# Kernel tuning notes

Measured on AMD Instinct MI355X. Metric: run time of the kernel, lower is better.

The kernel has to match this reference:

```python
import jax, jax.numpy as jnp
import numpy as np

N_NODES = 20000
N_EDGES = 640000
K_CHEB = 20


def setup_inputs() -> dict:
    key = jax.random.key(0)
    ks = jax.random.split(key, 8)
    x = jax.random.normal(ks[0], (128, N_NODES, 1), dtype=jnp.float32)
    rows = jax.random.randint(ks[1], (N_EDGES,), 0, N_NODES, dtype=jnp.int32)
    cols = jax.random.randint(ks[2], (N_EDGES,), 0, N_NODES, dtype=jnp.int32)
    # rescaled-Laplacian-like values, small scale so the K=20 recursion stays bounded
    vals = jax.random.normal(ks[3], (N_EDGES,), dtype=jnp.float32) * 0.05
    W_gc = jax.random.normal(ks[4], (K_CHEB, 10), dtype=jnp.float32) * 0.1
    b_gc = jnp.zeros((10,), dtype=jnp.float32)
    W_fc = jax.random.normal(ks[5], (N_NODES * 10, 10), dtype=jnp.float32) * 0.01
    b_fc = jnp.zeros((10,), dtype=jnp.float32)
    return {"x": x, "rows": rows, "cols": cols, "vals": vals,
            "W_gc": W_gc, "b_gc": b_gc, "W_fc": W_fc, "b_fc": b_fc}


def reference(x, rows, cols, vals, W_gc, b_gc, W_fc, b_fc):
    B, N, Fin = x.shape  # Fin == 1
    x0 = x[..., 0].T  # [N, B]

    def spmm(t):  # sparse L @ t via edge-list scatter-add, t: [N, B]
        return jax.ops.segment_sum(vals[:, None] * t[cols], rows, num_segments=N)

    # Chebyshev recursion: T0 = x, T1 = L x, Tk = 2 L T_{k-1} - T_{k-2}
    Ts = [x0, spmm(x0)]
    for _ in range(K_CHEB - 2):
        Ts.append(2.0 * spmm(Ts[-1]) - Ts[-2])
    Xt = jnp.stack(Ts, axis=-1)  # [N, B, K]

    gc = jnp.einsum('nbk,kf->bnf', Xt, W_gc) + b_gc  # [B, N, 10]
    gc = jax.nn.relu(gc)
    flat = gc.reshape(B, N * 10)
    h = jax.nn.relu(flat @ W_fc + b_fc)  # [B, 10]
    return jax.nn.softmax(h, axis=1)
```

## Files before the change

kernel.cpp:

```cpp
#include <hip/hip_runtime.h>
#include <hip/hip_bf16.h>
#include <hip/hip_fp16.h>
#include <math.h>


#define NF 10
#define KCHEB 20
#define BCG 64
#define COFF16 (KCHEB * BCG)

typedef unsigned int u32;


__global__ void init_kernel(int* counts, float* h_part, const float* __restrict__ W_gc,
                            float* __restrict__ WgT, int N, int H) {
    int i = blockIdx.x * blockDim.x + threadIdx.x;
    if (i < N) counts[i] = 0;
    if (i < H) h_part[i] = 0.f;
    if (i < KCHEB * NF) WgT[(i % NF) * KCHEB + (i / NF)] = W_gc[i];
}

__global__ void hist_kernel(const int* __restrict__ rows, int* __restrict__ counts, int E) {
    int e = blockIdx.x * blockDim.x + threadIdx.x;
    if (e < E) atomicAdd(&counts[rows[e]], 1);
}

#define SCAN_THREADS 1024
__global__ void scan_kernel(const int* __restrict__ counts, int* __restrict__ row_start,
                            int* __restrict__ cursor, int N) {
    __shared__ int sh[SCAN_THREADS];
    int t = threadIdx.x;
    int CH = (N + SCAN_THREADS - 1) / SCAN_THREADS;
    int base = t * CH;
    int sum = 0;
    for (int i = 0; i < CH; ++i) {
        int idx = base + i;
        sum += (idx < N) ? counts[idx] : 0;
    }
    sh[t] = sum;
    __syncthreads();
    for (int off = 1; off < SCAN_THREADS; off <<= 1) {
        int v = (t >= off) ? sh[t - off] : 0;
        __syncthreads();
        sh[t] += v;
        __syncthreads();
    }
    int run = (t == 0) ? 0 : sh[t - 1];
    for (int i = 0; i < CH; ++i) {
        int idx = base + i;
        if (idx < N) {
            int v = counts[idx];
            row_start[idx] = run;
            cursor[idx] = run;
            run += v;
        }
    }
    if (t == SCAN_THREADS - 1) row_start[N] = run;
}

__global__ void scatter_kernel(const int* __restrict__ rows, const int* __restrict__ cols,
                               const float* __restrict__ vals, int* __restrict__ cursor,
                               int2* __restrict__ csr, int E) {
    int e = blockIdx.x * blockDim.x + threadIdx.x;
    if (e >= E) return;
    int p = atomicAdd(&cursor[rows[e]], 1);
    csr[p] = make_int2(cols[e] * COFF16, __float_as_int(vals[e]));
}


__global__ void transpose_kernel(const float* __restrict__ x, __half* __restrict__ X16,
                                 float* __restrict__ C32, int N, int ntiles, int b0s) {
    __shared__ float tile[BCG][65];
    int tid = threadIdx.x;
    int g = blockIdx.x / ntiles;
    int ti = blockIdx.x - g * ntiles;
    int n0 = ti * 64;
#pragma unroll
    for (int p = 0; p < 16; ++p) {
        int idx = p * 256 + tid;
        int row = idx >> 6;
        int col = idx & 63;
        if (n0 + col < N)
            tile[row][col] = x[(size_t)(b0s + g * BCG + row) * N + n0 + col];
    }
    __syncthreads();
#pragma unroll
    for (int p = 0; p < 16; ++p) {
        int idx = p * 256 + tid;
        int nloc = idx >> 6;
        int bb = idx & 63;
        int n = n0 + nloc;
        if (n < N) {
            float v = tile[bb][nloc];
            X16[(size_t)(g * N + n) * COFF16 + bb] = __float2half_rn(v);
            C32[((size_t)(g * 2 + 0) * N + n) * BCG + bb] = v;
        }
    }
}


__global__ __launch_bounds__(256)
void spmm_kernel(__half* __restrict__ X16, float* __restrict__ C32,
                 const int* __restrict__ row_start, const int2* __restrict__ csr,
                 int N, int xpcShift, int subsPerChunk,
                 int kIn, int kOut, float alpha, float beta) {
    int xcd = blockIdx.x & 7;
    int chunk = xcd >> xpcShift;
    int xpcMask = (1 << xpcShift) - 1;
    int sub = (blockIdx.x >> 3) * (1 << xpcShift) + (xcd & xpcMask);
    if (sub >= subsPerChunk) return;
    int tid = threadIdx.x;
    int ln = tid >> 3;
    int bq = tid & 7;
    int n = sub * 32 + ln;
    if (n >= N) return;
    int s = row_start[n];
    int e = row_start[n + 1];

    const __half* gin = X16 + (size_t)chunk * N * COFF16;
    int koff = kIn * BCG + bq * 8;
    int bo = bq * 8;
    float acc[8];
#pragma unroll
    for (int q = 0; q < 8; ++q) acc[q] = 0.f;

    int i = s;
    for (; i + 4 <= e; i += 4) {
        int2 p0 = csr[i], p1 = csr[i + 1], p2 = csr[i + 2], p3 = csr[i + 3];
        uint4 u0 = *(const uint4*)(gin + p0.x + koff);
        uint4 u1 = *(const uint4*)(gin + p1.x + koff);
        uint4 u2 = *(const uint4*)(gin + p2.x + koff);
        uint4 u3 = *(const uint4*)(gin + p3.x + koff);
        float v0 = __int_as_float(p0.y), v1 = __int_as_float(p1.y);
        float v2 = __int_as_float(p2.y), v3 = __int_as_float(p3.y);
        {
            float2 f0 = __half22float2(*(__half2*)&u0.x), f1 = __half22float2(*(__half2*)&u0.y);
            float2 f2 = __half22float2(*(__half2*)&u0.z), f3 = __half22float2(*(__half2*)&u0.w);
            acc[0] += v0 * f0.x; acc[1] += v0 * f0.y; acc[2] += v0 * f1.x; acc[3] += v0 * f1.y;
            acc[4] += v0 * f2.x; acc[5] += v0 * f2.y; acc[6] += v0 * f3.x; acc[7] += v0 * f3.y;
        }
        {
            float2 f0 = __half22float2(*(__half2*)&u1.x), f1 = __half22float2(*(__half2*)&u1.y);
            float2 f2 = __half22float2(*(__half2*)&u1.z), f3 = __half22float2(*(__half2*)&u1.w);
            acc[0] += v1 * f0.x; acc[1] += v1 * f0.y; acc[2] += v1 * f1.x; acc[3] += v1 * f1.y;
            acc[4] += v1 * f2.x; acc[5] += v1 * f2.y; acc[6] += v1 * f3.x; acc[7] += v1 * f3.y;
        }
        {
            float2 f0 = __half22float2(*(__half2*)&u2.x), f1 = __half22float2(*(__half2*)&u2.y);
            float2 f2 = __half22float2(*(__half2*)&u2.z), f3 = __half22float2(*(__half2*)&u2.w);
            acc[0] += v2 * f0.x; acc[1] += v2 * f0.y; acc[2] += v2 * f1.x; acc[3] += v2 * f1.y;
            acc[4] += v2 * f2.x; acc[5] += v2 * f2.y; acc[6] += v2 * f3.x; acc[7] += v2 * f3.y;
        }
        {
            float2 f0 = __half22float2(*(__half2*)&u3.x), f1 = __half22float2(*(__half2*)&u3.y);
            float2 f2 = __half22float2(*(__half2*)&u3.z), f3 = __half22float2(*(__half2*)&u3.w);
            acc[0] += v3 * f0.x; acc[1] += v3 * f0.y; acc[2] += v3 * f1.x; acc[3] += v3 * f1.y;
            acc[4] += v3 * f2.x; acc[5] += v3 * f2.y; acc[6] += v3 * f3.x; acc[7] += v3 * f3.y;
        }
    }
    for (; i < e; ++i) {
        int2 p0 = csr[i];
        uint4 u0 = *(const uint4*)(gin + p0.x + koff);
        float v0 = __int_as_float(p0.y);
        float2 f0 = __half22float2(*(__half2*)&u0.x), f1 = __half22float2(*(__half2*)&u0.y);
        float2 f2 = __half22float2(*(__half2*)&u0.z), f3 = __half22float2(*(__half2*)&u0.w);
        acc[0] += v0 * f0.x; acc[1] += v0 * f0.y; acc[2] += v0 * f1.x; acc[3] += v0 * f1.y;
        acc[4] += v0 * f2.x; acc[5] += v0 * f2.y; acc[6] += v0 * f3.x; acc[7] += v0 * f3.y;
    }

    float* cslot = C32 + ((size_t)(chunk * 2 + (kOut & 1)) * N + n) * BCG + bo;
    float o[8];
#pragma unroll
    for (int q = 0; q < 8; ++q) o[q] = alpha * acc[q];
    if (beta != 0.f) {
        const float4 pv0 = *(const float4*)(cslot);
        const float4 pv1 = *(const float4*)(cslot + 4);
        o[0] += beta * pv0.x; o[1] += beta * pv0.y; o[2] += beta * pv0.z; o[3] += beta * pv0.w;
        o[4] += beta * pv1.x; o[5] += beta * pv1.y; o[6] += beta * pv1.z; o[7] += beta * pv1.w;
    }
    *(float4*)(cslot)     = make_float4(o[0], o[1], o[2], o[3]);
    *(float4*)(cslot + 4) = make_float4(o[4], o[5], o[6], o[7]);
    __half* o16 = X16 + (size_t)(chunk * N + n) * COFF16 + kOut * BCG + bo;
    uint4 h4;
    __half2 h01 = __floats2half2_rn(o[0], o[1]);
    __half2 h23 = __floats2half2_rn(o[2], o[3]);
    __half2 h45 = __floats2half2_rn(o[4], o[5]);
    __half2 h67 = __floats2half2_rn(o[6], o[7]);
    h4.x = *(u32*)&h01; h4.y = *(u32*)&h23; h4.z = *(u32*)&h45; h4.w = *(u32*)&h67;
    *(uint4*)o16 = h4;
}


__global__ __launch_bounds__(1024, 8)
void proj_fc_kernel(const __half* __restrict__ X16,
                    const float* __restrict__ WgT,
                    const float* __restrict__ b_gc,
                    const float* __restrict__ W_fc,
                    float* __restrict__ h_part,
                    int N, int b0s, int G) {
    __shared__ float sRed[BCG * 11];
    int tid = threadIdx.x;
    for (int i = tid; i < BCG * 11; i += 1024) sRed[i] = 0.f;
    __syncthreads();

    int g = blockIdx.x % G;
    int bidx = blockIdx.x / G;
    int nblk = gridDim.x / G;

    int bb = tid & (BCG - 1);
    int wv = __builtin_amdgcn_readfirstlane(tid >> 6);

    float h_loc[NF];
#pragma unroll
    for (int f = 0; f < NF; ++f) h_loc[f] = 0.f;

    const __half* chunkBase = X16 + (size_t)g * N * COFF16;
    int ngroups = (N + 15) / 16;
    for (int grp = bidx; grp < ngroups; grp += nblk) {
        int n = grp * 16 + wv;
        if (n < N) {
            float xt[KCHEB];
            const __half* xp = chunkBase + (size_t)n * COFF16 + bb;
#pragma unroll
            for (int k = 0; k < KCHEB; ++k) xt[k] = __half2float(xp[k * BCG]);

            const float* wfBase = W_fc + (size_t)n * (NF * NF);
#pragma unroll 1
            for (int j = 0; j < NF; ++j) {
                const float* wg = WgT + j * KCHEB;
                float gc = b_gc[j];
#pragma unroll
                for (int k = 0; k < KCHEB; ++k) gc += wg[k] * xt[k];
                gc = fmaxf(gc, 0.f);
                const float* wf = wfBase + j * NF;
#pragma unroll
                for (int f = 0; f < NF; ++f) h_loc[f] += gc * wf[f];
            }
        }
    }
#pragma unroll
    for (int f = 0; f < NF; ++f) atomicAdd(&sRed[bb * 11 + f], h_loc[f]);
    __syncthreads();
    for (int i = tid; i < BCG * NF; i += 1024) {
        int rb = i / NF;
        int rf = i - rb * NF;
        atomicAdd(&h_part[(size_t)(b0s + g * BCG + rb) * NF + rf], sRed[rb * 11 + rf]);
    }
}


__global__ void softmax_kernel(const float* __restrict__ h_part, const float* __restrict__ b_fc,
                               float* __restrict__ out, int B) {
    int b = blockIdx.x * blockDim.x + threadIdx.x;
    if (b >= B) return;
    float v[NF];
    float m = -1e30f;
#pragma unroll
    for (int f = 0; f < NF; ++f) {
        float t = fmaxf(h_part[b * NF + f] + b_fc[f], 0.f);
        v[f] = t;
        m = fmaxf(m, t);
    }
    float s = 0.f;
#pragma unroll
    for (int f = 0; f < NF; ++f) { v[f] = expf(v[f] - m); s += v[f]; }
    float inv = 1.f / s;
#pragma unroll
    for (int f = 0; f < NF; ++f) out[b * NF + f] = v[f] * inv;
}


extern "C" void kernel_launch(void* const* d_in, const int* in_sizes, int n_in,
                              void* d_out, int out_size, void* d_ws, size_t ws_size,
                              hipStream_t stream) {
    const float* x    = (const float*)d_in[0];
    const int*   rows = (const int*)d_in[1];
    const int*   cols = (const int*)d_in[2];
    const float* vals = (const float*)d_in[3];
    const float* W_gc = (const float*)d_in[4];
    const float* b_gc = (const float*)d_in[5];
    const float* W_fc = (const float*)d_in[6];
    const float* b_fc = (const float*)d_in[7];
    float* out = (float*)d_out;

    const int E = in_sizes[1];
    const int N = in_sizes[6] / (NF * NF);
    const int B = in_sizes[0] / N;

    char* p = (char*)d_ws;
    int* counts    = (int*)p;   p += sizeof(int) * (size_t)N;
    int* row_start = (int*)p;   p += sizeof(int) * (size_t)(N + 1);
    int* cursor    = (int*)p;   p += sizeof(int) * (size_t)N;
    p = (char*)(((size_t)p + 15) & ~(size_t)15);
    int2* csr      = (int2*)p;  p += sizeof(int2) * (size_t)E;
    float* h_part  = (float*)p; p += sizeof(float) * (size_t)B * NF;
    p = (char*)(((size_t)p + 15) & ~(size_t)15);
    float* WgT     = (float*)p; p += sizeof(float) * (size_t)(NF * KCHEB);
    size_t fixed = (size_t)(p - (char*)d_ws);
    fixed = (fixed + 255) & ~(size_t)255;

    size_t perChunk16 = (size_t)N * COFF16 * sizeof(__half);
    size_t perCarry   = (size_t)2 * N * BCG * sizeof(float);
    int G = (B >= 2 * BCG) ? 2 : 1;
    while (G > 1 && fixed + (size_t)G * (perChunk16 + perCarry) > ws_size) G >>= 1;
    __half* X16 = (__half*)((char*)d_ws + fixed);
    size_t x16b = ((size_t)G * perChunk16 + 255) & ~(size_t)255;
    float* C32 = (float*)((char*)d_ws + fixed + x16b);
    int xpcShift = (G == 2) ? 2 : 3;
    int BT = G * BCG;
    int nsc = B / BT;

    {
        int H = B * NF;
        int cov = (N > H) ? N : H;
        init_kernel<<<(cov + 255) / 256, 256, 0, stream>>>(counts, h_part, W_gc, WgT, N, H);
        hist_kernel<<<(E + 255) / 256, 256, 0, stream>>>(rows, counts, E);
        scan_kernel<<<1, SCAN_THREADS, 0, stream>>>(counts, row_start, cursor, N);
        scatter_kernel<<<(E + 255) / 256, 256, 0, stream>>>(rows, cols, vals, cursor, csr, E);
    }

    int ntiles = (N + 63) / 64;
    int subsPerChunk = (N + 31) / 32;
    int xpc = 1 << xpcShift;
    int gridSpmm = 8 * ((subsPerChunk + xpc - 1) / xpc);

    for (int c = 0; c < nsc; ++c) {
        int b0s = c * BT;
        transpose_kernel<<<G * ntiles, 256, 0, stream>>>(x, X16, C32, N, ntiles, b0s);
        for (int k = 1; k < KCHEB; ++k) {
            float alpha = (k == 1) ? 1.f : 2.f;
            float beta  = (k == 1) ? 0.f : -1.f;
            spmm_kernel<<<gridSpmm, 256, 0, stream>>>(
                X16, C32, row_start, csr, N, xpcShift, subsPerChunk,
                k - 1, k, alpha, beta);
        }
        proj_fc_kernel<<<256 * G, 1024, 0, stream>>>(X16, WgT, b_gc, W_fc, h_part, N, b0s, G);
    }

    softmax_kernel<<<1, 128, 0, stream>>>(h_part, b_fc, out, B);
}
```

Measured before the change: 597.5 us.

## Split SpMM into column-partitioned gather and partial-sum reduce kernels

The CSR is rebuilt so that edges are bucketed by column range as well as by row. This lets each XCD gather only from its own slice of the source features, shrinking the per-XCD gather working set for better L2 locality. Each gather writes per-slice partial sums to a new fp32 buffer with nontemporal stores. A second kernel then sums the slices and applies the Chebyshev alpha/beta update. The cost is an extra kernel launch per recursion step, plus writing and reading that partial buffer, which is several times the output size.

```diff
diff --git a/kernel.cpp b/kernel.cpp
--- a/kernel.cpp
+++ b/kernel.cpp
@@ -10,32 +10,37 @@
 #define COFF16 (KCHEB * BCG)
 
 typedef unsigned int u32;
+typedef float v4f __attribute__((ext_vector_type(4)));
 
 
 __global__ void init_kernel(int* counts, float* h_part, const float* __restrict__ W_gc,
-                            float* __restrict__ WgT, int N, int H) {
+                            float* __restrict__ WgT, int N4, int H) {
     int i = blockIdx.x * blockDim.x + threadIdx.x;
-    if (i < N) counts[i] = 0;
+    if (i < N4) counts[i] = 0;
     if (i < H) h_part[i] = 0.f;
     if (i < KCHEB * NF) WgT[(i % NF) * KCHEB + (i / NF)] = W_gc[i];
 }
 
-__global__ void hist_kernel(const int* __restrict__ rows, int* __restrict__ counts, int E) {
+__global__ void hist_kernel(const int* __restrict__ rows, const int* __restrict__ cols,
+                            int* __restrict__ counts, int E, int N, int QS) {
     int e = blockIdx.x * blockDim.x + threadIdx.x;
-    if (e < E) atomicAdd(&counts[rows[e]], 1);
+    if (e < E) {
+        int q = cols[e] / QS;
+        atomicAdd(&counts[q * N + rows[e]], 1);
+    }
 }
 
 #define SCAN_THREADS 1024
 __global__ void scan_kernel(const int* __restrict__ counts, int* __restrict__ row_start,
-                            int* __restrict__ cursor, int N) {
+                            int* __restrict__ cursor, int N4) {
     __shared__ int sh[SCAN_THREADS];
     int t = threadIdx.x;
-    int CH = (N + SCAN_THREADS - 1) / SCAN_THREADS;
+    int CH = (N4 + SCAN_THREADS - 1) / SCAN_THREADS;
     int base = t * CH;
     int sum = 0;
     for (int i = 0; i < CH; ++i) {
         int idx = base + i;
-        sum += (idx < N) ? counts[idx] : 0;
+        sum += (idx < N4) ? counts[idx] : 0;
     }
     sh[t] = sum;
     __syncthreads();
@@ -48,23 +53,25 @@
     int run = (t == 0) ? 0 : sh[t - 1];
     for (int i = 0; i < CH; ++i) {
         int idx = base + i;
-        if (idx < N) {
+        if (idx < N4) {
             int v = counts[idx];
             row_start[idx] = run;
             cursor[idx] = run;
             run += v;
         }
     }
-    if (t == SCAN_THREADS - 1) row_start[N] = run;
+    if (t == SCAN_THREADS - 1) row_start[N4] = run;
 }
 
 __global__ void scatter_kernel(const int* __restrict__ rows, const int* __restrict__ cols,
                                const float* __restrict__ vals, int* __restrict__ cursor,
-                               int2* __restrict__ csr, int E) {
+                               int2* __restrict__ csr, int E, int N, int QS) {
     int e = blockIdx.x * blockDim.x + threadIdx.x;
     if (e >= E) return;
-    int p = atomicAdd(&cursor[rows[e]], 1);
-    csr[p] = make_int2(cols[e] * COFF16, __float_as_int(vals[e]));
+    int col = cols[e];
+    int q = col / QS;
+    int p = atomicAdd(&cursor[q * N + rows[e]], 1);
+    csr[p] = make_int2(col * COFF16, __float_as_int(vals[e]));
 }
 
 
@@ -100,33 +107,32 @@
 
 
 __global__ __launch_bounds__(256)
-void spmm_kernel(__half* __restrict__ X16, float* __restrict__ C32,
-                 const int* __restrict__ row_start, const int2* __restrict__ csr,
-                 int N, int xpcShift, int subsPerChunk,
-                 int kIn, int kOut, float alpha, float beta) {
+void gather_kernel(const __half* __restrict__ X16, float* __restrict__ P,
+                   const int* __restrict__ row_start4, const int2* __restrict__ csr4,
+                   int N, int kIn, int nqMask, int nqSh, int gMask, int hSh, int twSh) {
     int xcd = blockIdx.x & 7;
-    int chunk = xcd >> xpcShift;
-    int xpcMask = (1 << xpcShift) - 1;
-    int sub = (blockIdx.x >> 3) * (1 << xpcShift) + (xcd & xpcMask);
-    if (sub >= subsPerChunk) return;
+    int sub = blockIdx.x >> 3;
+    int q = xcd & nqMask;
+    int c = (xcd >> nqSh) & gMask;
+    int h = xcd >> hSh;
     int tid = threadIdx.x;
     int ln = tid >> 3;
     int bq = tid & 7;
-    int n = sub * 32 + ln;
-    if (n >= N) return;
-    int s = row_start[n];
-    int e = row_start[n + 1];
-
-    const __half* gin = X16 + (size_t)chunk * N * COFF16;
+    int r = ((sub << twSh) + h) * 32 + ln;
+    if (r >= N) return;
+    int vr = q * N + r;
+    int s = row_start4[vr];
+    int e = row_start4[vr + 1];
+
+    const __half* gin = X16 + (size_t)c * N * COFF16;
     int koff = kIn * BCG + bq * 8;
-    int bo = bq * 8;
     float acc[8];
 #pragma unroll
-    for (int q = 0; q < 8; ++q) acc[q] = 0.f;
+    for (int t = 0; t < 8; ++t) acc[t] = 0.f;
 
     int i = s;
     for (; i + 4 <= e; i += 4) {
-        int2 p0 = csr[i], p1 = csr[i + 1], p2 = csr[i + 2], p3 = csr[i + 3];
+        int2 p0 = csr4[i], p1 = csr4[i + 1], p2 = csr4[i + 2], p3 = csr4[i + 3];
         uint4 u0 = *(const uint4*)(gin + p0.x + koff);
         uint4 u1 = *(const uint4*)(gin + p1.x + koff);
         uint4 u2 = *(const uint4*)(gin + p2.x + koff);
@@ -159,7 +165,7 @@
         }
     }
     for (; i < e; ++i) {
-        int2 p0 = csr[i];
+        int2 p0 = csr4[i];
         uint4 u0 = *(const uint4*)(gin + p0.x + koff);
         float v0 = __int_as_float(p0.y);
         float2 f0 = __half22float2(*(__half2*)&u0.x), f1 = __half22float2(*(__half2*)&u0.y);
@@ -168,10 +174,47 @@
         acc[4] += v0 * f2.x; acc[5] += v0 * f2.y; acc[6] += v0 * f3.x; acc[7] += v0 * f3.y;
     }
 
-    float* cslot = C32 + ((size_t)(chunk * 2 + (kOut & 1)) * N + n) * BCG + bo;
+    float* pp = P + ((size_t)((c << nqSh) + q) * N + r) * BCG + bq * 8;
+    v4f a0 = { acc[0], acc[1], acc[2], acc[3] };
+    v4f a1 = { acc[4], acc[5], acc[6], acc[7] };
+    __builtin_nontemporal_store(a0, (v4f*)pp);
+    __builtin_nontemporal_store(a1, (v4f*)(pp + 4));
+}
+
+
+__global__ __launch_bounds__(256)
+void reduce_kernel(__half* __restrict__ X16, float* __restrict__ C32,
+                   const float* __restrict__ P,
+                   int N, int QS, int NQ, int nqMask, int nqSh, int gMask, int hSh, int twSh,
+                   int kOut, float alpha, float beta) {
+    int xcd = blockIdx.x & 7;
+    int sub = blockIdx.x >> 3;
+    int q = xcd & nqMask;
+    int c = (xcd >> nqSh) & gMask;
+    int h = xcd >> hSh;
+    int tid = threadIdx.x;
+    int ln = tid >> 3;
+    int bq = tid & 7;
+    int r = q * QS + ((sub << twSh) + h) * 32 + ln;
+    int rend = (q + 1) * QS; if (rend > N) rend = N;
+    if (r >= rend) return;
+    int bo = bq * 8;
+
+    float acc[8];
+#pragma unroll
+    for (int t = 0; t < 8; ++t) acc[t] = 0.f;
+    for (int qq = 0; qq < NQ; ++qq) {
+        const float* pp = P + ((size_t)((c << nqSh) + qq) * N + r) * BCG + bo;
+        v4f a0 = __builtin_nontemporal_load((const v4f*)pp);
+        v4f a1 = __builtin_nontemporal_load((const v4f*)(pp + 4));
+        acc[0] += a0.x; acc[1] += a0.y; acc[2] += a0.z; acc[3] += a0.w;
+        acc[4] += a1.x; acc[5] += a1.y; acc[6] += a1.z; acc[7] += a1.w;
+    }
+
+    float* cslot = C32 + ((size_t)(c * 2 + (kOut & 1)) * N + r) * BCG + bo;
     float o[8];
 #pragma unroll
-    for (int q = 0; q < 8; ++q) o[q] = alpha * acc[q];
+    for (int t = 0; t < 8; ++t) o[t] = alpha * acc[t];
     if (beta != 0.f) {
         const float4 pv0 = *(const float4*)(cslot);
         const float4 pv1 = *(const float4*)(cslot + 4);
@@ -180,7 +223,7 @@
     }
     *(float4*)(cslot)     = make_float4(o[0], o[1], o[2], o[3]);
     *(float4*)(cslot + 4) = make_float4(o[4], o[5], o[6], o[7]);
-    __half* o16 = X16 + (size_t)(chunk * N + n) * COFF16 + kOut * BCG + bo;
+    __half* o16 = X16 + (size_t)(c * N + r) * COFF16 + kOut * BCG + bo;
     uint4 h4;
     __half2 h01 = __floats2half2_rn(o[0], o[1]);
     __half2 h23 = __floats2half2_rn(o[2], o[3]);
@@ -269,6 +312,8 @@
     for (int f = 0; f < NF; ++f) out[b * NF + f] = v[f] * inv;
 }
 
+
+static inline int ilog2i(int v) { int s = 0; while ((1 << s) < v) ++s; return s; }
 
 extern "C" void kernel_launch(void* const* d_in, const int* in_sizes, int n_in,
                               void* d_out, int out_size, void* d_ws, size_t ws_size,
@@ -288,9 +333,9 @@
     const int B = in_sizes[0] / N;
 
     char* p = (char*)d_ws;
-    int* counts    = (int*)p;   p += sizeof(int) * (size_t)N;
-    int* row_start = (int*)p;   p += sizeof(int) * (size_t)(N + 1);
-    int* cursor    = (int*)p;   p += sizeof(int) * (size_t)N;
+    int* counts    = (int*)p;   p += sizeof(int) * (size_t)(8 * N);
+    int* row_start = (int*)p;   p += sizeof(int) * (size_t)(8 * N + 1);
+    int* cursor    = (int*)p;   p += sizeof(int) * (size_t)(8 * N);
     p = (char*)(((size_t)p + 15) & ~(size_t)15);
     int2* csr      = (int2*)p;  p += sizeof(int2) * (size_t)E;
     float* h_part  = (float*)p; p += sizeof(float) * (size_t)B * NF;
@@ -301,28 +346,47 @@
 
     size_t perChunk16 = (size_t)N * COFF16 * sizeof(__half);
     size_t perCarry   = (size_t)2 * N * BCG * sizeof(float);
+    size_t perP       = (size_t)N * BCG * sizeof(float);
+
     int G = (B >= 2 * BCG) ? 2 : 1;
-    while (G > 1 && fixed + (size_t)G * (perChunk16 + perCarry) > ws_size) G >>= 1;
+    int NQ = (G == 2) ? 2 : 8;
+    while (fixed + (size_t)G * (perChunk16 + perCarry) + (size_t)G * NQ * perP > ws_size) {
+        if (G == 2) { G = 1; NQ = 8; }
+        else if (NQ > 1) { NQ >>= 1; }
+        else break;
+    }
     __half* X16 = (__half*)((char*)d_ws + fixed);
     size_t x16b = ((size_t)G * perChunk16 + 255) & ~(size_t)255;
     float* C32 = (float*)((char*)d_ws + fixed + x16b);
-    int xpcShift = (G == 2) ? 2 : 3;
+    size_t c32b = ((size_t)G * perCarry + 255) & ~(size_t)255;
+    float* P = (float*)((char*)d_ws + fixed + x16b + c32b);
+
     int BT = G * BCG;
     int nsc = B / BT;
+    int QS = (N + NQ - 1) / NQ;
+    int N4 = NQ * N;
+    int TW = 8 / (G * NQ);
+    int nqSh = ilog2i(NQ);
+    int gSh  = ilog2i(G);
+    int twSh = ilog2i(TW);
+    int hSh  = nqSh + gSh;
+    int nqMask = NQ - 1;
+    int gMask  = G - 1;
 
     {
         int H = B * NF;
-        int cov = (N > H) ? N : H;
-        init_kernel<<<(cov + 255) / 256, 256, 0, stream>>>(counts, h_part, W_gc, WgT, N, H);
-        hist_kernel<<<(E + 255) / 256, 256, 0, stream>>>(rows, counts, E);
-        scan_kernel<<<1, SCAN_THREADS, 0, stream>>>(counts, row_start, cursor, N);
-        scatter_kernel<<<(E + 255) / 256, 256, 0, stream>>>(rows, cols, vals, cursor, csr, E);
+        int cov = (N4 > H) ? N4 : H;
+        init_kernel<<<(cov + 255) / 256, 256, 0, stream>>>(counts, h_part, W_gc, WgT, N4, H);
+        hist_kernel<<<(E + 255) / 256, 256, 0, stream>>>(rows, cols, counts, E, N, QS);
+        scan_kernel<<<1, SCAN_THREADS, 0, stream>>>(counts, row_start, cursor, N4);
+        scatter_kernel<<<(E + 255) / 256, 256, 0, stream>>>(rows, cols, vals, cursor, csr, E, N, QS);
     }
 
     int ntiles = (N + 63) / 64;
-    int subsPerChunk = (N + 31) / 32;
-    int xpc = 1 << xpcShift;
-    int gridSpmm = 8 * ((subsPerChunk + xpc - 1) / xpc);
+    int subsG = (N + 32 * TW - 1) / (32 * TW);
+    int subsR = (QS + 32 * TW - 1) / (32 * TW);
+    int gridGather = 8 * subsG;
+    int gridReduce = 8 * subsR;
 
     for (int c = 0; c < nsc; ++c) {
         int b0s = c * BT;
@@ -330,9 +394,11 @@
         for (int k = 1; k < KCHEB; ++k) {
             float alpha = (k == 1) ? 1.f : 2.f;
             float beta  = (k == 1) ? 0.f : -1.f;
-            spmm_kernel<<<gridSpmm, 256, 0, stream>>>(
-                X16, C32, row_start, csr, N, xpcShift, subsPerChunk,
-                k - 1, k, alpha, beta);
+            gather_kernel<<<gridGather, 256, 0, stream>>>(
+                X16, P, row_start, csr, N, k - 1, nqMask, nqSh, gMask, hSh, twSh);
+            reduce_kernel<<<gridReduce, 256, 0, stream>>>(
+                X16, C32, P, N, QS, NQ, nqMask, nqSh, gMask, hSh, twSh,
+                k, alpha, beta);
         }
         proj_fc_kernel<<<256 * G, 1024, 0, stream>>>(X16, WgT, b_gc, W_fc, h_part, N, b0s, G);
     }
```

Result: slower. 822.4 us (+37.6%).

## Split batch into eight 16-wide XCD chunks with packed 32-bit CSR entries

Applied to the files above, without the earlier changes.

Reorganizes the working set so the 128 batch columns are split into 8 chunks of 16. Each chunk maps to one XCD (blockIdx & 7), and the layout is per-k planar rather than interleaved. Each chunk's working set is smaller, so the gather it drives should stay inside one XCD's L2. CSR entries are packed into 32 bits: a 16-bit column index plus a half-precision value. Carry and CSR accesses use nontemporal loads and stores. Risks: the 16-bit column only holds N up to 65536, fp16 edge values lose precision, and each gathered row is now only 32 bytes.

```diff
diff --git a/kernel.cpp b/kernel.cpp
--- a/kernel.cpp
+++ b/kernel.cpp
@@ -6,10 +6,11 @@
 
 #define NF 10
 #define KCHEB 20
-#define BCG 64
-#define COFF16 (KCHEB * BCG)
+#define BCG 16
+#define NCH 8
 
 typedef unsigned int u32;
+typedef float v4f __attribute__((ext_vector_type(4)));
 
 
 __global__ void init_kernel(int* counts, float* h_part, const float* __restrict__ W_gc,
@@ -60,40 +61,59 @@
 
 __global__ void scatter_kernel(const int* __restrict__ rows, const int* __restrict__ cols,
                                const float* __restrict__ vals, int* __restrict__ cursor,
-                               int2* __restrict__ csr, int E) {
+                               u32* __restrict__ csr, int E) {
     int e = blockIdx.x * blockDim.x + threadIdx.x;
     if (e >= E) return;
     int p = atomicAdd(&cursor[rows[e]], 1);
-    csr[p] = make_int2(cols[e] * COFF16, __float_as_int(vals[e]));
+    __half hv = __float2half_rn(vals[e]);
+    csr[p] = ((u32)cols[e] << 16) | (u32)__half_as_ushort(hv);
 }
 
 
 __global__ void transpose_kernel(const float* __restrict__ x, __half* __restrict__ X16,
-                                 float* __restrict__ C32, int N, int ntiles, int b0s) {
-    __shared__ float tile[BCG][65];
+                                 float* __restrict__ C32, int N, int b0s) {
+    __shared__ float tile[128][65];
     int tid = threadIdx.x;
-    int g = blockIdx.x / ntiles;
-    int ti = blockIdx.x - g * ntiles;
-    int n0 = ti * 64;
-#pragma unroll
-    for (int p = 0; p < 16; ++p) {
+    int n0 = blockIdx.x * 64;
+#pragma unroll
+    for (int p = 0; p < 32; ++p) {
         int idx = p * 256 + tid;
-        int row = idx >> 6;
-        int col = idx & 63;
-        if (n0 + col < N)
-            tile[row][col] = x[(size_t)(b0s + g * BCG + row) * N + n0 + col];
+        int bl = idx >> 6;
+        int nl = idx & 63;
+        if (n0 + nl < N)
+            tile[bl][nl] = x[(size_t)(b0s + bl) * N + n0 + nl];
     }
     __syncthreads();
 #pragma unroll
-    for (int p = 0; p < 16; ++p) {
+    for (int p = 0; p < 4; ++p) {
         int idx = p * 256 + tid;
-        int nloc = idx >> 6;
-        int bb = idx & 63;
-        int n = n0 + nloc;
+        int cc = idx >> 7;
+        int nl = (idx >> 1) & 63;
+        int hf = idx & 1;
+        int n = n0 + nl;
         if (n < N) {
-            float v = tile[bb][nloc];
-            X16[(size_t)(g * N + n) * COFF16 + bb] = __float2half_rn(v);
-            C32[((size_t)(g * 2 + 0) * N + n) * BCG + bb] = v;
+            __half hbuf[8];
+#pragma unroll
+            for (int q = 0; q < 8; ++q)
+                hbuf[q] = __float2half_rn(tile[cc * 16 + hf * 8 + q][nl]);
+            *(uint4*)(X16 + ((size_t)cc * KCHEB + 0) * N * 16 + (size_t)n * 16 + hf * 8) =
+                *(uint4*)hbuf;
+        }
+    }
+#pragma unroll
+    for (int p = 0; p < 8; ++p) {
+        int idx = p * 256 + tid;
+        int cc = idx >> 8;
+        int rem = idx & 255;
+        int nl = rem >> 2;
+        int qd = rem & 3;
+        int n = n0 + nl;
+        if (n < N) {
+            float4 f4 = make_float4(tile[cc * 16 + qd * 4 + 0][nl],
+                                    tile[cc * 16 + qd * 4 + 1][nl],
+                                    tile[cc * 16 + qd * 4 + 2][nl],
+                                    tile[cc * 16 + qd * 4 + 3][nl]);
+            *(float4*)(C32 + ((size_t)cc * 2 + 0) * N * 16 + (size_t)n * 16 + qd * 4) = f4;
         }
     }
 }
@@ -101,38 +121,38 @@
 
 __global__ __launch_bounds__(256)
 void spmm_kernel(__half* __restrict__ X16, float* __restrict__ C32,
-                 const int* __restrict__ row_start, const int2* __restrict__ csr,
-                 int N, int xpcShift, int subsPerChunk,
-                 int kIn, int kOut, float alpha, float beta) {
-    int xcd = blockIdx.x & 7;
-    int chunk = xcd >> xpcShift;
-    int xpcMask = (1 << xpcShift) - 1;
-    int sub = (blockIdx.x >> 3) * (1 << xpcShift) + (xcd & xpcMask);
-    if (sub >= subsPerChunk) return;
+                 const int* __restrict__ row_start, const u32* __restrict__ csr,
+                 int N, int kIn, int kOut, float alpha, float beta) {
+    int c = blockIdx.x & 7;
+    int sub = blockIdx.x >> 3;
     int tid = threadIdx.x;
-    int ln = tid >> 3;
-    int bq = tid & 7;
-    int n = sub * 32 + ln;
+    int ln = tid >> 1;
+    int hf = tid & 1;
+    int n = sub * 128 + ln;
     if (n >= N) return;
     int s = row_start[n];
     int e = row_start[n + 1];
 
-    const __half* gin = X16 + (size_t)chunk * N * COFF16;
-    int koff = kIn * BCG + bq * 8;
-    int bo = bq * 8;
+    const __half* gin = X16 + ((size_t)c * KCHEB + kIn) * N * 16;
+    int bo = hf * 8;
     float acc[8];
 #pragma unroll
     for (int q = 0; q < 8; ++q) acc[q] = 0.f;
 
     int i = s;
     for (; i + 4 <= e; i += 4) {
-        int2 p0 = csr[i], p1 = csr[i + 1], p2 = csr[i + 2], p3 = csr[i + 3];
-        uint4 u0 = *(const uint4*)(gin + p0.x + koff);
-        uint4 u1 = *(const uint4*)(gin + p1.x + koff);
-        uint4 u2 = *(const uint4*)(gin + p2.x + koff);
-        uint4 u3 = *(const uint4*)(gin + p3.x + koff);
-        float v0 = __int_as_float(p0.y), v1 = __int_as_float(p1.y);
-        float v2 = __int_as_float(p2.y), v3 = __int_as_float(p3.y);
+        u32 pv0 = __builtin_nontemporal_load(csr + i);
+        u32 pv1 = __builtin_nontemporal_load(csr + i + 1);
+        u32 pv2 = __builtin_nontemporal_load(csr + i + 2);
+        u32 pv3 = __builtin_nontemporal_load(csr + i + 3);
+        uint4 u0 = *(const uint4*)(gin + (size_t)(pv0 >> 16) * 16 + bo);
+        uint4 u1 = *(const uint4*)(gin + (size_t)(pv1 >> 16) * 16 + bo);
+        uint4 u2 = *(const uint4*)(gin + (size_t)(pv2 >> 16) * 16 + bo);
+        uint4 u3 = *(const uint4*)(gin + (size_t)(pv3 >> 16) * 16 + bo);
+        float v0 = __half2float(__ushort_as_half((unsigned short)(pv0 & 0xffffu)));
+        float v1 = __half2float(__ushort_as_half((unsigned short)(pv1 & 0xffffu)));
+        float v2 = __half2float(__ushort_as_half((unsigned short)(pv2 & 0xffffu)));
+        float v3 = __half2float(__ushort_as_half((unsigned short)(pv3 & 0xffffu)));
         {
             float2 f0 = __half22float2(*(__half2*)&u0.x), f1 = __half22float2(*(__half2*)&u0.y);
             float2 f2 = __half22float2(*(__half2*)&u0.z), f3 = __half22float2(*(__half2*)&u0.w);
@@ -159,35 +179,37 @@
         }
     }
     for (; i < e; ++i) {
-        int2 p0 = csr[i];
-        uint4 u0 = *(const uint4*)(gin + p0.x + koff);
-        float v0 = __int_as_float(p0.y);
+        u32 pv0 = __builtin_nontemporal_load(csr + i);
+        uint4 u0 = *(const uint4*)(gin + (size_t)(pv0 >> 16) * 16 + bo);
+        float v0 = __half2float(__ushort_as_half((unsigned short)(pv0 & 0xffffu)));
         float2 f0 = __half22float2(*(__half2*)&u0.x), f1 = __half22float2(*(__half2*)&u0.y);
         float2 f2 = __half22float2(*(__half2*)&u0.z), f3 = __half22float2(*(__half2*)&u0.w);
         acc[0] += v0 * f0.x; acc[1] += v0 * f0.y; acc[2] += v0 * f1.x; acc[3] += v0 * f1.y;
         acc[4] += v0 * f2.x; acc[5] += v0 * f2.y; acc[6] += v0 * f3.x; acc[7] += v0 * f3.y;
     }
 
-    float* cslot = C32 + ((size_t)(chunk * 2 + (kOut & 1)) * N + n) * BCG + bo;
+    float* cs = C32 + (((size_t)c * 2 + (kOut & 1)) * N + n) * 16 + bo;
     float o[8];
 #pragma unroll
     for (int q = 0; q < 8; ++q) o[q] = alpha * acc[q];
     if (beta != 0.f) {
-        const float4 pv0 = *(const float4*)(cslot);
-        const float4 pv1 = *(const float4*)(cslot + 4);
+        v4f pv0 = __builtin_nontemporal_load((const v4f*)cs);
+        v4f pv1 = __builtin_nontemporal_load((const v4f*)(cs + 4));
         o[0] += beta * pv0.x; o[1] += beta * pv0.y; o[2] += beta * pv0.z; o[3] += beta * pv0.w;
         o[4] += beta * pv1.x; o[5] += beta * pv1.y; o[6] += beta * pv1.z; o[7] += beta * pv1.w;
     }
-    *(float4*)(cslot)     = make_float4(o[0], o[1], o[2], o[3]);
-    *(float4*)(cslot + 4) = make_float4(o[4], o[5], o[6], o[7]);
-    __half* o16 = X16 + (size_t)(chunk * N + n) * COFF16 + kOut * BCG + bo;
+    v4f s0 = { o[0], o[1], o[2], o[3] };
+    v4f s1 = { o[4], o[5], o[6], o[7] };
+    __builtin_nontemporal_store(s0, (v4f*)cs);
+    __builtin_nontemporal_store(s1, (v4f*)(cs + 4));
+    __half* oo = X16 + ((size_t)c * KCHEB + kOut) * N * 16 + (size_t)n * 16 + bo;
     uint4 h4;
     __half2 h01 = __floats2half2_rn(o[0], o[1]);
     __half2 h23 = __floats2half2_rn(o[2], o[3]);
     __half2 h45 = __floats2half2_rn(o[4], o[5]);
     __half2 h67 = __floats2half2_rn(o[6], o[7]);
     h4.x = *(u32*)&h01; h4.y = *(u32*)&h23; h4.z = *(u32*)&h45; h4.w = *(u32*)&h67;
-    *(uint4*)o16 = h4;
+    *(uint4*)oo = h4;
 }
 
 
@@ -197,32 +219,33 @@
                     const float* __restrict__ b_gc,
                     const float* __restrict__ W_fc,
                     float* __restrict__ h_part,
-                    int N, int b0s, int G) {
-    __shared__ float sRed[BCG * 11];
+                    int N, int b0s) {
+    __shared__ float sRed[128 * 11];
     int tid = threadIdx.x;
-    for (int i = tid; i < BCG * 11; i += 1024) sRed[i] = 0.f;
+    for (int i = tid; i < 128 * 11; i += 1024) sRed[i] = 0.f;
     __syncthreads();
 
-    int g = blockIdx.x % G;
-    int bidx = blockIdx.x / G;
-    int nblk = gridDim.x / G;
-
-    int bb = tid & (BCG - 1);
+    int lane = tid & 63;
+    int bb = lane & 15;
+    int lg = lane >> 4;
     int wv = __builtin_amdgcn_readfirstlane(tid >> 6);
+    int nslot = wv >> 1;
+    int g0 = (wv & 1) * 4;
+    int g = g0 + lg;
+    int b = g * 16 + bb;
 
     float h_loc[NF];
 #pragma unroll
     for (int f = 0; f < NF; ++f) h_loc[f] = 0.f;
 
-    const __half* chunkBase = X16 + (size_t)g * N * COFF16;
-    int ngroups = (N + 15) / 16;
-    for (int grp = bidx; grp < ngroups; grp += nblk) {
-        int n = grp * 16 + wv;
+    int ngroups = (N + 7) / 8;
+    for (int grp = blockIdx.x; grp < ngroups; grp += gridDim.x) {
+        int n = grp * 8 + nslot;
         if (n < N) {
             float xt[KCHEB];
-            const __half* xp = chunkBase + (size_t)n * COFF16 + bb;
-#pragma unroll
-            for (int k = 0; k < KCHEB; ++k) xt[k] = __half2float(xp[k * BCG]);
+#pragma unroll
+            for (int k = 0; k < KCHEB; ++k)
+                xt[k] = __half2float(X16[((size_t)g * KCHEB + k) * N * 16 + (size_t)n * 16 + bb]);
 
             const float* wfBase = W_fc + (size_t)n * (NF * NF);
 #pragma unroll 1
@@ -239,12 +262,12 @@
         }
     }
 #pragma unroll
-    for (int f = 0; f < NF; ++f) atomicAdd(&sRed[bb * 11 + f], h_loc[f]);
+    for (int f = 0; f < NF; ++f) atomicAdd(&sRed[b * 11 + f], h_loc[f]);
     __syncthreads();
-    for (int i = tid; i < BCG * NF; i += 1024) {
+    for (int i = tid; i < 128 * NF; i += 1024) {
         int rb = i / NF;
         int rf = i - rb * NF;
-        atomicAdd(&h_part[(size_t)(b0s + g * BCG + rb) * NF + rf], sRed[rb * 11 + rf]);
+        atomicAdd(&h_part[(size_t)(b0s + rb) * NF + rf], sRed[rb * 11 + rf]);
     }
 }
 
@@ -292,23 +315,20 @@
     int* row_start = (int*)p;   p += sizeof(int) * (size_t)(N + 1);
     int* cursor    = (int*)p;   p += sizeof(int) * (size_t)N;
     p = (char*)(((size_t)p + 15) & ~(size_t)15);
-    int2* csr      = (int2*)p;  p += sizeof(int2) * (size_t)E;
+    u32* csr       = (u32*)p;   p += sizeof(u32) * (size_t)E;
     float* h_part  = (float*)p; p += sizeof(float) * (size_t)B * NF;
     p = (char*)(((size_t)p + 15) & ~(size_t)15);
     float* WgT     = (float*)p; p += sizeof(float) * (size_t)(NF * KCHEB);
     size_t fixed = (size_t)(p - (char*)d_ws);
     fixed = (fixed + 255) & ~(size_t)255;
 
-    size_t perChunk16 = (size_t)N * COFF16 * sizeof(__half);
-    size_t perCarry   = (size_t)2 * N * BCG * sizeof(float);
-    int G = (B >= 2 * BCG) ? 2 : 1;
-    while (G > 1 && fixed + (size_t)G * (perChunk16 + perCarry) > ws_size) G >>= 1;
     __half* X16 = (__half*)((char*)d_ws + fixed);
-    size_t x16b = ((size_t)G * perChunk16 + 255) & ~(size_t)255;
+    size_t x16b = ((size_t)NCH * KCHEB * N * 16 * sizeof(__half) + 255) & ~(size_t)255;
     float* C32 = (float*)((char*)d_ws + fixed + x16b);
-    int xpcShift = (G == 2) ? 2 : 3;
-    int BT = G * BCG;
+
+    int BT = NCH * BCG;
     int nsc = B / BT;
+    if (nsc < 1) nsc = 1;
 
     {
         int H = B * NF;
@@ -320,21 +340,19 @@
     }
 
     int ntiles = (N + 63) / 64;
-    int subsPerChunk = (N + 31) / 32;
-    int xpc = 1 << xpcShift;
-    int gridSpmm = 8 * ((subsPerChunk + xpc - 1) / xpc);
+    int subs = (N + 127) / 128;
+    int gridSpmm = 8 * subs;
 
     for (int c = 0; c < nsc; ++c) {
         int b0s = c * BT;
-        transpose_kernel<<<G * ntiles, 256, 0, stream>>>(x, X16, C32, N, ntiles, b0s);
+        transpose_kernel<<<ntiles, 256, 0, stream>>>(x, X16, C32, N, b0s);
         for (int k = 1; k < KCHEB; ++k) {
             float alpha = (k == 1) ? 1.f : 2.f;
             float beta  = (k == 1) ? 0.f : -1.f;
             spmm_kernel<<<gridSpmm, 256, 0, stream>>>(
-                X16, C32, row_start, csr, N, xpcShift, subsPerChunk,
-                k - 1, k, alpha, beta);
-        }
-        proj_fc_kernel<<<256 * G, 1024, 0, stream>>>(X16, WgT, b_gc, W_fc, h_part, N, b0s, G);
+                X16, C32, row_start, csr, N, k - 1, k, alpha, beta);
+        }
+        proj_fc_kernel<<<512, 1024, 0, stream>>>(X16, WgT, b_gc, W_fc, h_part, N, b0s);
     }
 
     softmax_kernel<<<1, 128, 0, stream>>>(h_part, b_fc, out, B);
```

Result: slower. 1.264 ms (+111.5%).

## Split batch into four 32-wide chunks per XCD pair with nontemporal SpMM loads

Applied to the files above, without the earlier changes.

Shrinks each batch chunk from 64 to 32 columns and raises the chunk count to four, so that each chunk maps onto fewer XCDs. The intent is that each XCD's L2 holds a smaller gather working set during the SpMM recursion. The SpMM now gathers 8-byte half vectors per thread, and the CSR stream and fp32 carry use nontemporal loads and stores to avoid polluting the cache. The projection kernel is restructured to cover all four chunks inside one block. The trade-off is narrower gathers, and therefore more CSR index reads per useful byte.

```diff
diff --git a/kernel.cpp b/kernel.cpp
--- a/kernel.cpp
+++ b/kernel.cpp
@@ -6,10 +6,12 @@
 
 #define NF 10
 #define KCHEB 20
-#define BCG 64
+#define BCG 32
 #define COFF16 (KCHEB * BCG)
 
 typedef unsigned int u32;
+typedef float v4f __attribute__((ext_vector_type(4)));
+typedef u32 v2u __attribute__((ext_vector_type(2)));
 
 
 __global__ void init_kernel(int* counts, float* h_part, const float* __restrict__ W_gc,
@@ -76,7 +78,7 @@
     int ti = blockIdx.x - g * ntiles;
     int n0 = ti * 64;
 #pragma unroll
-    for (int p = 0; p < 16; ++p) {
+    for (int p = 0; p < 8; ++p) {
         int idx = p * 256 + tid;
         int row = idx >> 6;
         int col = idx & 63;
@@ -85,10 +87,10 @@
     }
     __syncthreads();
 #pragma unroll
-    for (int p = 0; p < 16; ++p) {
+    for (int p = 0; p < 8; ++p) {
         int idx = p * 256 + tid;
-        int nloc = idx >> 6;
-        int bb = idx & 63;
+        int nloc = idx >> 5;
+        int bb = idx & 31;
         int n = n0 + nloc;
         if (n < N) {
             float v = tile[bb][nloc];
@@ -118,76 +120,65 @@
     int e = row_start[n + 1];
 
     const __half* gin = X16 + (size_t)chunk * N * COFF16;
-    int koff = kIn * BCG + bq * 8;
-    int bo = bq * 8;
-    float acc[8];
-#pragma unroll
-    for (int q = 0; q < 8; ++q) acc[q] = 0.f;
+    int koff = kIn * BCG + bq * 4;
+    int bo = bq * 4;
+    float acc[4];
+#pragma unroll
+    for (int q = 0; q < 4; ++q) acc[q] = 0.f;
 
     int i = s;
     for (; i + 4 <= e; i += 4) {
-        int2 p0 = csr[i], p1 = csr[i + 1], p2 = csr[i + 2], p3 = csr[i + 3];
-        uint4 u0 = *(const uint4*)(gin + p0.x + koff);
-        uint4 u1 = *(const uint4*)(gin + p1.x + koff);
-        uint4 u2 = *(const uint4*)(gin + p2.x + koff);
-        uint4 u3 = *(const uint4*)(gin + p3.x + koff);
-        float v0 = __int_as_float(p0.y), v1 = __int_as_float(p1.y);
-        float v2 = __int_as_float(p2.y), v3 = __int_as_float(p3.y);
+        v2u c0 = __builtin_nontemporal_load((const v2u*)(csr + i));
+        v2u c1 = __builtin_nontemporal_load((const v2u*)(csr + i + 1));
+        v2u c2 = __builtin_nontemporal_load((const v2u*)(csr + i + 2));
+        v2u c3 = __builtin_nontemporal_load((const v2u*)(csr + i + 3));
+        uint2 u0 = *(const uint2*)(gin + (int)c0.x + koff);
+        uint2 u1 = *(const uint2*)(gin + (int)c1.x + koff);
+        uint2 u2 = *(const uint2*)(gin + (int)c2.x + koff);
+        uint2 u3 = *(const uint2*)(gin + (int)c3.x + koff);
+        float v0 = __int_as_float((int)c0.y), v1 = __int_as_float((int)c1.y);
+        float v2 = __int_as_float((int)c2.y), v3 = __int_as_float((int)c3.y);
         {
             float2 f0 = __half22float2(*(__half2*)&u0.x), f1 = __half22float2(*(__half2*)&u0.y);
-            float2 f2 = __half22float2(*(__half2*)&u0.z), f3 = __half22float2(*(__half2*)&u0.w);
             acc[0] += v0 * f0.x; acc[1] += v0 * f0.y; acc[2] += v0 * f1.x; acc[3] += v0 * f1.y;
-            acc[4] += v0 * f2.x; acc[5] += v0 * f2.y; acc[6] += v0 * f3.x; acc[7] += v0 * f3.y;
         }
         {
             float2 f0 = __half22float2(*(__half2*)&u1.x), f1 = __half22float2(*(__half2*)&u1.y);
-            float2 f2 = __half22float2(*(__half2*)&u1.z), f3 = __half22float2(*(__half2*)&u1.w);
             acc[0] += v1 * f0.x; acc[1] += v1 * f0.y; acc[2] += v1 * f1.x; acc[3] += v1 * f1.y;
-            acc[4] += v1 * f2.x; acc[5] += v1 * f2.y; acc[6] += v1 * f3.x; acc[7] += v1 * f3.y;
         }
         {
             float2 f0 = __half22float2(*(__half2*)&u2.x), f1 = __half22float2(*(__half2*)&u2.y);
-            float2 f2 = __half22float2(*(__half2*)&u2.z), f3 = __half22float2(*(__half2*)&u2.w);
             acc[0] += v2 * f0.x; acc[1] += v2 * f0.y; acc[2] += v2 * f1.x; acc[3] += v2 * f1.y;
-            acc[4] += v2 * f2.x; acc[5] += v2 * f2.y; acc[6] += v2 * f3.x; acc[7] += v2 * f3.y;
         }
         {
             float2 f0 = __half22float2(*(__half2*)&u3.x), f1 = __half22float2(*(__half2*)&u3.y);
-            float2 f2 = __half22float2(*(__half2*)&u3.z), f3 = __half22float2(*(__half2*)&u3.w);
             acc[0] += v3 * f0.x; acc[1] += v3 * f0.y; acc[2] += v3 * f1.x; acc[3] += v3 * f1.y;
-            acc[4] += v3 * f2.x; acc[5] += v3 * f2.y; acc[6] += v3 * f3.x; acc[7] += v3 * f3.y;
         }
     }
     for (; i < e; ++i) {
-        int2 p0 = csr[i];
-        uint4 u0 = *(const uint4*)(gin + p0.x + koff);
-        float v0 = __int_as_float(p0.y);
+        v2u c0 = __builtin_nontemporal_load((const v2u*)(csr + i));
+        uint2 u0 = *(const uint2*)(gin + (int)c0.x + koff);
+        float v0 = __int_as_float((int)c0.y);
         float2 f0 = __half22float2(*(__half2*)&u0.x), f1 = __half22float2(*(__half2*)&u0.y);
-        float2 f2 = __half22float2(*(__half2*)&u0.z), f3 = __half22float2(*(__half2*)&u0.w);
         acc[0] += v0 * f0.x; acc[1] += v0 * f0.y; acc[2] += v0 * f1.x; acc[3] += v0 * f1.y;
-        acc[4] += v0 * f2.x; acc[5] += v0 * f2.y; acc[6] += v0 * f3.x; acc[7] += v0 * f3.y;
     }
 
     float* cslot = C32 + ((size_t)(chunk * 2 + (kOut & 1)) * N + n) * BCG + bo;
-    float o[8];
-#pragma unroll
-    for (int q = 0; q < 8; ++q) o[q] = alpha * acc[q];
+    float o[4];
+#pragma unroll
+    for (int q = 0; q < 4; ++q) o[q] = alpha * acc[q];
     if (beta != 0.f) {
-        const float4 pv0 = *(const float4*)(cslot);
-        const float4 pv1 = *(const float4*)(cslot + 4);
-        o[0] += beta * pv0.x; o[1] += beta * pv0.y; o[2] += beta * pv0.z; o[3] += beta * pv0.w;
-        o[4] += beta * pv1.x; o[5] += beta * pv1.y; o[6] += beta * pv1.z; o[7] += beta * pv1.w;
-    }
-    *(float4*)(cslot)     = make_float4(o[0], o[1], o[2], o[3]);
-    *(float4*)(cslot + 4) = make_float4(o[4], o[5], o[6], o[7]);
+        v4f pv = __builtin_nontemporal_load((const v4f*)cslot);
+        o[0] += beta * pv.x; o[1] += beta * pv.y; o[2] += beta * pv.z; o[3] += beta * pv.w;
+    }
+    v4f sv = { o[0], o[1], o[2], o[3] };
+    __builtin_nontemporal_store(sv, (v4f*)cslot);
     __half* o16 = X16 + (size_t)(chunk * N + n) * COFF16 + kOut * BCG + bo;
-    uint4 h4;
+    uint2 h2;
     __half2 h01 = __floats2half2_rn(o[0], o[1]);
     __half2 h23 = __floats2half2_rn(o[2], o[3]);
-    __half2 h45 = __floats2half2_rn(o[4], o[5]);
-    __half2 h67 = __floats2half2_rn(o[6], o[7]);
-    h4.x = *(u32*)&h01; h4.y = *(u32*)&h23; h4.z = *(u32*)&h45; h4.w = *(u32*)&h67;
-    *(uint4*)o16 = h4;
+    h2.x = *(u32*)&h01; h2.y = *(u32*)&h23;
+    *(uint2*)o16 = h2;
 }
 
 
@@ -197,30 +188,31 @@
                     const float* __restrict__ b_gc,
                     const float* __restrict__ W_fc,
                     float* __restrict__ h_part,
-                    int N, int b0s, int G) {
-    __shared__ float sRed[BCG * 11];
+                    int N, int b0s) {
+    __shared__ float sRed[128 * 11];
     int tid = threadIdx.x;
-    for (int i = tid; i < BCG * 11; i += 1024) sRed[i] = 0.f;
+    for (int i = tid; i < 128 * 11; i += 1024) sRed[i] = 0.f;
     __syncthreads();
 
-    int g = blockIdx.x % G;
-    int bidx = blockIdx.x / G;
-    int nblk = gridDim.x / G;
-
-    int bb = tid & (BCG - 1);
+    int lane = tid & 63;
+    int bb = lane & (BCG - 1);
+    int lg = lane >> 5;
     int wv = __builtin_amdgcn_readfirstlane(tid >> 6);
+    int nslot = wv >> 1;
+    int g0 = (wv & 1) * 2;
+    int g = g0 + lg;
+    int b = g * BCG + bb;
 
     float h_loc[NF];
 #pragma unroll
     for (int f = 0; f < NF; ++f) h_loc[f] = 0.f;
 
-    const __half* chunkBase = X16 + (size_t)g * N * COFF16;
-    int ngroups = (N + 15) / 16;
-    for (int grp = bidx; grp < ngroups; grp += nblk) {
-        int n = grp * 16 + wv;
+    int ngroups = (N + 7) / 8;
+    for (int grp = blockIdx.x; grp < ngroups; grp += gridDim.x) {
+        int n = grp * 8 + nslot;
         if (n < N) {
             float xt[KCHEB];
-            const __half* xp = chunkBase + (size_t)n * COFF16 + bb;
+            const __half* xp = X16 + (size_t)(g * N + n) * COFF16 + bb;
 #pragma unroll
             for (int k = 0; k < KCHEB; ++k) xt[k] = __half2float(xp[k * BCG]);
 
@@ -239,12 +231,12 @@
         }
     }
 #pragma unroll
-    for (int f = 0; f < NF; ++f) atomicAdd(&sRed[bb * 11 + f], h_loc[f]);
+    for (int f = 0; f < NF; ++f) atomicAdd(&sRed[b * 11 + f], h_loc[f]);
     __syncthreads();
-    for (int i = tid; i < BCG * NF; i += 1024) {
+    for (int i = tid; i < 128 * NF; i += 1024) {
         int rb = i / NF;
         int rf = i - rb * NF;
-        atomicAdd(&h_part[(size_t)(b0s + g * BCG + rb) * NF + rf], sRed[rb * 11 + rf]);
+        atomicAdd(&h_part[(size_t)(b0s + rb) * NF + rf], sRed[rb * 11 + rf]);
     }
 }
 
@@ -269,6 +261,8 @@
     for (int f = 0; f < NF; ++f) out[b * NF + f] = v[f] * inv;
 }
 
+
+static inline int ilog2i(int v) { int s = 0; while ((1 << s) < v) ++s; return s; }
 
 extern "C" void kernel_launch(void* const* d_in, const int* in_sizes, int n_in,
                               void* d_out, int out_size, void* d_ws, size_t ws_size,
@@ -301,14 +295,15 @@
 
     size_t perChunk16 = (size_t)N * COFF16 * sizeof(__half);
     size_t perCarry   = (size_t)2 * N * BCG * sizeof(float);
-    int G = (B >= 2 * BCG) ? 2 : 1;
+    int G = (B >= 4 * BCG) ? 4 : ((B >= 2 * BCG) ? 2 : 1);
     while (G > 1 && fixed + (size_t)G * (perChunk16 + perCarry) > ws_size) G >>= 1;
     __half* X16 = (__half*)((char*)d_ws + fixed);
     size_t x16b = ((size_t)G * perChunk16 + 255) & ~(size_t)255;
     float* C32 = (float*)((char*)d_ws + fixed + x16b);
-    int xpcShift = (G == 2) ? 2 : 3;
+    int xpcShift = 3 - ilog2i(G);
     int BT = G * BCG;
     int nsc = B / BT;
+    if (nsc < 1) nsc = 1;
 
     {
         int H = B * NF;
@@ -334,7 +329,7 @@
                 X16, C32, row_start, csr, N, xpcShift, subsPerChunk,
                 k - 1, k, alpha, beta);
         }
-        proj_fc_kernel<<<256 * G, 1024, 0, stream>>>(X16, WgT, b_gc, W_fc, h_part, N, b0s, G);
+        proj_fc_kernel<<<512, 1024, 0, stream>>>(X16, WgT, b_gc, W_fc, h_part, N, b0s);
     }
 
     softmax_kernel<<<1, 128, 0, stream>>>(h_part, b_fc, out, B);
```

After: 1.198 ms. 100% more time.
